# Performance work log

Hardware: AMD Instinct MI355X
Metric: run time of the kernel (lower is better)

Reference implementation:

```python
import jax, jax.numpy as jnp
import numpy as np

N_HEADS = 16


def setup_inputs() -> dict:
    key = jax.random.key(0)
    k1, k2 = jax.random.split(key)
    bs, width, length = 8, 3 * N_HEADS * 64, 1024  # C=64 per head
    qkv = jax.random.normal(k1, (bs, width, length), dtype=jnp.float32)
    mask = jax.random.uniform(k2, (bs, length), dtype=jnp.float32)
    return {"qkv": qkv, "mask": mask}


def reference(qkv, mask):
    bs, width, length = qkv.shape
    ch = width // (3 * N_HEADS)
    q, k, v = jnp.split(qkv, 3, axis=1)
    # view(bs*H, ch, T): head index is inner (b*H + h ordering)
    q = q.reshape(bs * N_HEADS, ch, length)
    k = k.reshape(bs * N_HEADS, ch, length)
    v = v.reshape(bs * N_HEADS, ch, length)
    scale = 1.0 / jnp.sqrt(jnp.sqrt(jnp.asarray(ch, dtype=qkv.dtype)))
    # [bs*H, T, T] score matrix
    weight = jnp.einsum('bct,bcs->bts', q * scale, k * scale)
    # torch mask.repeat(n_heads, 1) tiles the batch dim -> jnp.tile
    m = jnp.tile(mask, (N_HEADS, 1))[:, None, :]  # [bs*H, 1, T]
    weight = weight * m
    weight = jax.nn.softmax(weight.astype(jnp.float32), axis=-1).astype(weight.dtype)
    a = jnp.einsum('bts,bcs->bct', weight, v)  # [bs*H, ch, T]
    return a.reshape(bs, N_HEADS * ch, length)
```

## Files before the change

kernel.cpp:

```cpp
#include <hip/hip_runtime.h>
#include <stdint.h>
#include <math.h>

typedef float  f32x4  __attribute__((ext_vector_type(4)));
typedef __bf16 bf16x8 __attribute__((ext_vector_type(8)));
typedef __bf16 bf16x4 __attribute__((ext_vector_type(4)));

#define MFMA16(a, b, c) __builtin_amdgcn_mfma_f32_16x16x32_bf16((a), (b), (c), 0, 0, 0)
#define EXP2(x) __builtin_amdgcn_exp2f(x)

static constexpr int kT = 1024;

static constexpr int kTileEl = 4096;
static constexpr size_t kTensorEl    = (size_t)128 * 16 * kTileEl;
static constexpr size_t kTensorBytes = kTensorEl * 2;

static constexpr int kLS = 72;

__device__ inline void async16(const void* g, void* l) {
  __builtin_amdgcn_global_load_lds(
      (const __attribute__((address_space(1))) void*)g,
      (__attribute__((address_space(3))) void*)l, 16, 0, 0);
}

__global__ __launch_bounds__(256, 8)
void prepass(const float* __restrict__ qkv, const float* __restrict__ mask,
             __bf16* __restrict__ kh, __bf16* __restrict__ vh)
{
  __shared__ float ts[64 * 65];
  const int tid = threadIdx.x;
  const int bid = blockIdx.x, bh = bid >> 4, tile = bid & 15;
  const int b = bh >> 4, h = bh & 15, t0 = tile * 64;
  const float* __restrict__ kb = qkv + (size_t)(b * 3072 + 1024 + h * 64) * kT;
  const float* __restrict__ vb = qkv + (size_t)(b * 3072 + 2048 + h * 64) * kT;
  const float* __restrict__ mrow = mask + (size_t)(h & 7) * kT;
  const size_t tbase = ((size_t)bh * 16 + tile) * kTileEl;

  const int t4   = (tid & 15) * 4;
  const int crow = tid >> 4;
  const f32x4 m4 = *(const f32x4*)&mrow[t0 + t4];
  #pragma unroll
  for (int i = 0; i < 4; ++i) {
    const int c = i * 16 + crow;
    f32x4 k4 = *(const f32x4*)&kb[(size_t)c * kT + t0 + t4];
    k4 *= m4;
    *(f32x4*)&ts[c * 65 + t4] = k4;
  }
  __syncthreads();

  #pragma unroll
  for (int i = 0; i < 2; ++i) {
    const int p = i * 256 + tid;
    const int chunk = p >> 6, pl = p & 63;
    const int vc  = (chunk >> 1) * 16 + (pl & 15);
    const int vs0 = (chunk & 1) * 32 + (pl >> 4) * 8;
    const f32x4 va  = *(const f32x4*)&vb[(size_t)vc * kT + t0 + vs0];
    const f32x4 vbq = *(const f32x4*)&vb[(size_t)vc * kT + t0 + vs0 + 4];
    const int ks  = (chunk >> 1) * 16 + (pl & 15);
    const int kc0 = (chunk & 1) * 32 + (pl >> 4) * 8;
    bf16x8 k8, v8;
    #pragma unroll
    for (int j = 0; j < 8; ++j) k8[j] = (__bf16)ts[(kc0 + j) * 65 + ks];
    #pragma unroll
    for (int j = 0; j < 4; ++j) { v8[j] = (__bf16)va[j]; v8[4 + j] = (__bf16)vbq[j]; }
    *(bf16x8*)&kh[tbase + (size_t)p * 8] = k8;
    *(bf16x8*)&vh[tbase + (size_t)p * 8] = v8;
  }
}

__global__ __launch_bounds__(256, 5)
void attn_main(const float* __restrict__ qkv,
               const __bf16* __restrict__ kh, const __bf16* __restrict__ vh,
               float* __restrict__ out)
{
  __shared__ __align__(16) char smem[24576];

  const int tid  = threadIdx.x;
  const int lane = tid & 63;
  const int wave = tid >> 6;
  const int quad = lane >> 4;
  const int l15  = lane & 15;

  const int bid = blockIdx.x;
  const int bh  = bid & 127;
  const int tt  = bid >> 7;
  const int b   = bh >> 4;
  const int h   = bh & 15;
  const int t0  = tt * 64;
  const size_t hbase = (size_t)bh * 16;

  bf16x8 qh[2], ql[2];
  {
    float* ts = (float*)smem;
    const float* __restrict__ qb = qkv + (size_t)(b * 3072 + h * 64) * kT;
    const int t4   = (tid & 15) * 4;
    const int crow = tid >> 4;
    #pragma unroll
    for (int i = 0; i < 4; ++i) {
      const int c = i * 16 + crow;
      f32x4 q4 = *(const f32x4*)&qb[(size_t)c * kT + t0 + t4];
      q4 *= 0.18033688f;
      *(f32x4*)&ts[c * 65 + t4] = q4;
    }
    __syncthreads();
    const int trow = wave * 16 + l15;
    #pragma unroll
    for (int kc = 0; kc < 2; ++kc) {
      bf16x8 hf, lf;
      #pragma unroll
      for (int j = 0; j < 8; ++j) {
        float q = ts[(kc * 32 + quad * 8 + j) * 65 + trow];
        __bf16 hi = (__bf16)q;
        hf[j] = hi;
        lf[j] = (__bf16)(q - (float)hi);
      }
      qh[kc] = hf;
      ql[kc] = lf;
    }
    __syncthreads();
  }

  {
    const char* g = (const char*)(kh + hbase * kTileEl) + (size_t)lane * 16;
    for (int i = wave; i < 8; i += 4) async16(g + i * 1024, smem + i * 1024);
  }

  f32x4 O[4];
  #pragma unroll
  for (int cc = 0; cc < 4; ++cc) O[cc] = (f32x4){0.f, 0.f, 0.f, 0.f};
  float lsum = 0.f;

  char* sPw = smem + 16384 + wave * 2048;
  const int pwr = (l15 << 4) + ((quad & 1) << 3) + ((quad >> 1) << 8);

  for (int st = 0; st < 16; ++st) {
    __syncthreads();

    const __bf16* __restrict__ vt = vh + (hbase + st) * kTileEl;

    bf16x8 vf0[4], vf1[4];
    #pragma unroll
    for (int cc = 0; cc < 4; ++cc)
      vf0[cc] = *(const bf16x8*)&vt[(size_t)(cc * 2) * 512 + lane * 8];

    if (st < 15) {
      const char* g = (const char*)(kh + (hbase + st + 1) * kTileEl) + (size_t)lane * 16;
      char* l = smem + ((st + 1) & 1) * 8192;
      for (int i = wave; i < 8; i += 4) async16(g + i * 1024, l + i * 1024);
    }

    const __bf16* __restrict__ sKc = (const __bf16*)(smem + (st & 1) * 8192);

    #pragma unroll
    for (int sc = 0; sc < 4; ++sc) {
      bf16x8 k0 = *(const bf16x8*)&sKc[(size_t)(sc * 2) * 512 + lane * 8];
      bf16x8 k1 = *(const bf16x8*)&sKc[(size_t)(sc * 2 + 1) * 512 + lane * 8];
      f32x4 a = (f32x4){0.f, 0.f, 0.f, 0.f};
      a = MFMA16(k0, ql[0], a);
      a = MFMA16(k0, qh[0], a);
      a = MFMA16(k1, ql[1], a);
      a = MFMA16(k1, qh[1], a);
      bf16x4 p;
      #pragma unroll
      for (int r = 0; r < 4; ++r) {
        float e = EXP2(a[r]);
        lsum += e;
        p[r] = (__bf16)e;
      }
      *(bf16x4*)(sPw + (((sc >> 1) << 10) + ((sc & 1) << 9) + pwr)) = p;
    }

    #pragma unroll
    for (int cc = 0; cc < 4; ++cc)
      vf1[cc] = *(const bf16x8*)&vt[(size_t)(cc * 2 + 1) * 512 + lane * 8];

    bf16x8 pb0 = *(const bf16x8*)(sPw + lane * 16);
    bf16x8 pb1 = *(const bf16x8*)(sPw + 1024 + lane * 16);

    #pragma unroll
    for (int cc = 0; cc < 4; ++cc) {
      O[cc] = MFMA16(vf0[cc], pb0, O[cc]);
      O[cc] = MFMA16(vf1[cc], pb1, O[cc]);
    }
  }

  lsum += __shfl_xor(lsum, 16);
  lsum += __shfl_xor(lsum, 32);
  const float inv = 1.0f / lsum;

  const int tcol = t0 + wave * 16 + l15;
  float* __restrict__ obase = out + (size_t)b * (1024 * 1024) + (size_t)(h * 64) * kT;
  #pragma unroll
  for (int cc = 0; cc < 4; ++cc) {
    #pragma unroll
    for (int r = 0; r < 4; ++r) {
      obase[(size_t)(cc * 16 + quad * 4 + r) * kT + tcol] = O[cc][r] * inv;
    }
  }
}

__global__ __launch_bounds__(256, 2)
void attn_fused(const float* __restrict__ qkv, const float* __restrict__ mask,
                float* __restrict__ out)
{
  __shared__ __align__(16) __bf16 Ahi[64 * kLS];
  __shared__ __align__(16) __bf16 Alo[64 * kLS];
  __shared__ __align__(16) __bf16 Vhi[64 * kLS];
  __shared__ __align__(16) __bf16 Vlo[64 * kLS];
  __shared__ __align__(16) __bf16 Phi[64 * kLS];
  __shared__ __align__(16) __bf16 Plo[64 * kLS];
  __shared__ __align__(16) float  ms[64];

  const int tid  = threadIdx.x;
  const int lane = tid & 63;
  const int wave = tid >> 6;
  const int quad = lane >> 4;
  const int l15  = lane & 15;

  const int bid = blockIdx.x;
  const int bh  = bid >> 4;
  const int tb  = bid & 15;
  const int b   = bh >> 4;
  const int h   = bh & 15;
  const int t0  = tb * 64;

  const float* __restrict__ qbase = qkv + (size_t)(b * 3072 + h * 64) * kT;
  const float* __restrict__ kbase = qkv + (size_t)(b * 3072 + 1024 + h * 64) * kT;
  const float* __restrict__ vbase = qkv + (size_t)(b * 3072 + 2048 + h * 64) * kT;
  const float* __restrict__ mrow  = mask + (size_t)(h & 7) * kT;

  const int sl = tid & 63;
  const int cg = tid >> 6;

  #pragma unroll
  for (int i = 0; i < 16; ++i) {
    const int c = cg * 16 + i;
    float v  = qbase[(size_t)c * kT + t0 + sl] * 0.125f;
    __bf16 hi = (__bf16)v;
    Ahi[sl * kLS + c] = hi;
    Alo[sl * kLS + c] = (__bf16)(v - (float)hi);
  }
  __syncthreads();

  bf16x8 qh[2], ql[2];
  {
    const int row = (wave * 16 + l15) * kLS;
    #pragma unroll
    for (int kc = 0; kc < 2; ++kc) {
      qh[kc] = *(const bf16x8*)&Ahi[row + kc * 32 + quad * 8];
      ql[kc] = *(const bf16x8*)&Alo[row + kc * 32 + quad * 8];
    }
  }
  __syncthreads();

  f32x4 O[4];
  #pragma unroll
  for (int cc = 0; cc < 4; ++cc) O[cc] = (f32x4){0.f, 0.f, 0.f, 0.f};
  float m_run = -__builtin_inff();
  float l_run = 0.f;

  for (int s0 = 0; s0 < kT; s0 += 64) {
    #pragma unroll
    for (int i = 0; i < 16; ++i) {
      const int c = cg * 16 + i;
      float kv   = kbase[(size_t)c * kT + s0 + sl];
      __bf16 khi = (__bf16)kv;
      Ahi[sl * kLS + c] = khi;
      Alo[sl * kLS + c] = (__bf16)(kv - (float)khi);
      float vv   = vbase[(size_t)c * kT + s0 + sl];
      __bf16 vhi = (__bf16)vv;
      Vhi[c * kLS + sl] = vhi;
      Vlo[c * kLS + sl] = (__bf16)(vv - (float)vhi);
    }
    if (tid < 64) ms[tid] = mrow[s0 + tid];
    __syncthreads();

    f32x4 S[4];
    #pragma unroll
    for (int sc = 0; sc < 4; ++sc) {
      f32x4 acc = (f32x4){0.f, 0.f, 0.f, 0.f};
      #pragma unroll
      for (int kc = 0; kc < 2; ++kc) {
        const int off = (sc * 16 + l15) * kLS + kc * 32 + quad * 8;
        bf16x8 kh8 = *(const bf16x8*)&Ahi[off];
        bf16x8 kl8 = *(const bf16x8*)&Alo[off];
        acc = MFMA16(kh8, ql[kc], acc);
        acc = MFMA16(kl8, qh[kc], acc);
        acc = MFMA16(kh8, qh[kc], acc);
      }
      S[sc] = acc;
    }

    float x[16];
    float tmax = -__builtin_inff();
    #pragma unroll
    for (int sc = 0; sc < 4; ++sc) {
      f32x4 mv = *(const f32x4*)&ms[sc * 16 + quad * 4];
      #pragma unroll
      for (int r = 0; r < 4; ++r) {
        float xv = S[sc][r] * mv[r];
        x[sc * 4 + r] = xv;
        tmax = fmaxf(tmax, xv);
      }
    }
    tmax = fmaxf(tmax, __shfl_xor(tmax, 16));
    tmax = fmaxf(tmax, __shfl_xor(tmax, 32));
    const float mnew  = fmaxf(m_run, tmax);
    const float alpha = __expf(m_run - mnew);
    float tsum = 0.f;
    #pragma unroll
    for (int i = 0; i < 16; ++i) {
      float p = __expf(x[i] - mnew);
      x[i] = p;
      tsum += p;
    }
    tsum += __shfl_xor(tsum, 16);
    tsum += __shfl_xor(tsum, 32);
    l_run = l_run * alpha + tsum;
    m_run = mnew;
    #pragma unroll
    for (int cc = 0; cc < 4; ++cc) O[cc] = O[cc] * alpha;

    const int prow = (wave * 16 + l15) * kLS;
    #pragma unroll
    for (int sc = 0; sc < 4; ++sc) {
      bf16x4 ph, pl;
      #pragma unroll
      for (int r = 0; r < 4; ++r) {
        float p   = x[sc * 4 + r];
        __bf16 hi = (__bf16)p;
        ph[r] = hi;
        pl[r] = (__bf16)(p - (float)hi);
      }
      *(bf16x4*)&Phi[prow + sc * 16 + quad * 4] = ph;
      *(bf16x4*)&Plo[prow + sc * 16 + quad * 4] = pl;
    }
    __syncthreads();

    bf16x8 pbh[2], pbl[2];
    #pragma unroll
    for (int kc = 0; kc < 2; ++kc) {
      pbh[kc] = *(const bf16x8*)&Phi[prow + kc * 32 + quad * 8];
      pbl[kc] = *(const bf16x8*)&Plo[prow + kc * 32 + quad * 8];
    }
    #pragma unroll
    for (int cc = 0; cc < 4; ++cc) {
      #pragma unroll
      for (int kc = 0; kc < 2; ++kc) {
        const int off = (cc * 16 + l15) * kLS + kc * 32 + quad * 8;
        bf16x8 v8 = *(const bf16x8*)&Vhi[off];
        bf16x8 w8 = *(const bf16x8*)&Vlo[off];
        O[cc] = MFMA16(v8, pbl[kc], O[cc]);
        O[cc] = MFMA16(w8, pbh[kc], O[cc]);
        O[cc] = MFMA16(v8, pbh[kc], O[cc]);
      }
    }
    __syncthreads();
  }

  const float inv  = 1.0f / l_run;
  const int   tcol = t0 + wave * 16 + l15;
  float* __restrict__ obase = out + (size_t)b * (1024 * 1024) + (size_t)(h * 64) * kT;
  #pragma unroll
  for (int cc = 0; cc < 4; ++cc) {
    #pragma unroll
    for (int r = 0; r < 4; ++r) {
      const int c = cc * 16 + quad * 4 + r;
      obase[(size_t)c * kT + tcol] = O[cc][r] * inv;
    }
  }
}

extern "C" void kernel_launch(void* const* d_in, const int* in_sizes, int n_in,
                              void* d_out, int out_size, void* d_ws, size_t ws_size,
                              hipStream_t stream)
{
  const float* qkv  = (const float*)d_in[0];
  const float* mask = (const float*)d_in[1];
  float* out = (float*)d_out;
  (void)in_sizes; (void)n_in; (void)out_size;

  if (ws_size >= 2 * kTensorBytes) {
    char* w = (char*)d_ws;
    __bf16* kh = (__bf16*)(w + 0 * kTensorBytes);
    __bf16* vh = (__bf16*)(w + 1 * kTensorBytes);
    prepass<<<dim3(2048), dim3(256), 0, stream>>>(qkv, mask, kh, vh);
    attn_main<<<dim3(2048), dim3(256), 0, stream>>>(qkv, kh, vh, out);
  } else {
    attn_fused<<<dim3(2048), dim3(256), 0, stream>>>(qkv, mask, out);
  }
}
```

Baseline: 214.7 us.

## Process two 64-query tiles per block to reuse K/V loads

```diff
diff --git a/kernel.cpp b/kernel.cpp
--- a/kernel.cpp
+++ b/kernel.cpp
@@ -68,12 +68,12 @@
   }
 }
 
-__global__ __launch_bounds__(256, 5)
+__global__ __launch_bounds__(256, 4)
 void attn_main(const float* __restrict__ qkv,
                const __bf16* __restrict__ kh, const __bf16* __restrict__ vh,
                float* __restrict__ out)
 {
-  __shared__ __align__(16) char smem[24576];
+  __shared__ __align__(16) char smem[32768];
 
   const int tid  = threadIdx.x;
   const int lane = tid & 63;
@@ -83,41 +83,45 @@
 
   const int bid = blockIdx.x;
   const int bh  = bid & 127;
-  const int tt  = bid >> 7;
+  const int tp  = bid >> 7;
   const int b   = bh >> 4;
   const int h   = bh & 15;
-  const int t0  = tt * 64;
+  const int t0  = tp * 128;
   const size_t hbase = (size_t)bh * 16;
 
-  bf16x8 qh[2], ql[2];
+  bf16x8 qh[2][2], ql[2][2];
   {
     float* ts = (float*)smem;
     const float* __restrict__ qb = qkv + (size_t)(b * 3072 + h * 64) * kT;
     const int t4   = (tid & 15) * 4;
     const int crow = tid >> 4;
-    #pragma unroll
-    for (int i = 0; i < 4; ++i) {
-      const int c = i * 16 + crow;
-      f32x4 q4 = *(const f32x4*)&qb[(size_t)c * kT + t0 + t4];
-      q4 *= 0.18033688f;
-      *(f32x4*)&ts[c * 65 + t4] = q4;
-    }
-    __syncthreads();
     const int trow = wave * 16 + l15;
     #pragma unroll
-    for (int kc = 0; kc < 2; ++kc) {
-      bf16x8 hf, lf;
-      #pragma unroll
-      for (int j = 0; j < 8; ++j) {
-        float q = ts[(kc * 32 + quad * 8 + j) * 65 + trow];
-        __bf16 hi = (__bf16)q;
-        hf[j] = hi;
-        lf[j] = (__bf16)(q - (float)hi);
-      }
-      qh[kc] = hf;
-      ql[kc] = lf;
-    }
-    __syncthreads();
+    for (int half = 0; half < 2; ++half) {
+      const int tq0 = t0 + half * 64;
+      #pragma unroll
+      for (int i = 0; i < 4; ++i) {
+        const int c = i * 16 + crow;
+        f32x4 q4 = *(const f32x4*)&qb[(size_t)c * kT + tq0 + t4];
+        q4 *= 0.18033688f;
+        *(f32x4*)&ts[c * 65 + t4] = q4;
+      }
+      __syncthreads();
+      #pragma unroll
+      for (int kc = 0; kc < 2; ++kc) {
+        bf16x8 hf, lf;
+        #pragma unroll
+        for (int j = 0; j < 8; ++j) {
+          float q = ts[(kc * 32 + quad * 8 + j) * 65 + trow];
+          __bf16 hi = (__bf16)q;
+          hf[j] = hi;
+          lf[j] = (__bf16)(q - (float)hi);
+        }
+        qh[half][kc] = hf;
+        ql[half][kc] = lf;
+      }
+      __syncthreads();
+    }
   }
 
   {
@@ -125,12 +129,16 @@
     for (int i = wave; i < 8; i += 4) async16(g + i * 1024, smem + i * 1024);
   }
 
-  f32x4 O[4];
-  #pragma unroll
-  for (int cc = 0; cc < 4; ++cc) O[cc] = (f32x4){0.f, 0.f, 0.f, 0.f};
-  float lsum = 0.f;
-
-  char* sPw = smem + 16384 + wave * 2048;
+  f32x4 O0[4], O1[4];
+  #pragma unroll
+  for (int cc = 0; cc < 4; ++cc) {
+    O0[cc] = (f32x4){0.f, 0.f, 0.f, 0.f};
+    O1[cc] = (f32x4){0.f, 0.f, 0.f, 0.f};
+  }
+  float ls0 = 0.f, ls1 = 0.f;
+
+  char* sP0 = smem + 16384 + wave * 4096;
+  char* sP1 = sP0 + 2048;
   const int pwr = (l15 << 4) + ((quad & 1) << 3) + ((quad >> 1) << 8);
 
   for (int st = 0; st < 16; ++st) {
@@ -151,42 +159,63 @@
 
     const __bf16* __restrict__ sKc = (const __bf16*)(smem + (st & 1) * 8192);
 
+    __builtin_amdgcn_s_setprio(1);
+
     #pragma unroll
     for (int sc = 0; sc < 4; ++sc) {
       bf16x8 k0 = *(const bf16x8*)&sKc[(size_t)(sc * 2) * 512 + lane * 8];
       bf16x8 k1 = *(const bf16x8*)&sKc[(size_t)(sc * 2 + 1) * 512 + lane * 8];
-      f32x4 a = (f32x4){0.f, 0.f, 0.f, 0.f};
-      a = MFMA16(k0, ql[0], a);
-      a = MFMA16(k0, qh[0], a);
-      a = MFMA16(k1, ql[1], a);
-      a = MFMA16(k1, qh[1], a);
-      bf16x4 p;
+      f32x4 a0 = (f32x4){0.f, 0.f, 0.f, 0.f};
+      f32x4 a1 = (f32x4){0.f, 0.f, 0.f, 0.f};
+      a0 = MFMA16(k0, ql[0][0], a0);
+      a1 = MFMA16(k0, ql[1][0], a1);
+      a0 = MFMA16(k0, qh[0][0], a0);
+      a1 = MFMA16(k0, qh[1][0], a1);
+      a0 = MFMA16(k1, ql[0][1], a0);
+      a1 = MFMA16(k1, ql[1][1], a1);
+      a0 = MFMA16(k1, qh[0][1], a0);
+      a1 = MFMA16(k1, qh[1][1], a1);
+      bf16x4 p0, p1;
       #pragma unroll
       for (int r = 0; r < 4; ++r) {
-        float e = EXP2(a[r]);
-        lsum += e;
-        p[r] = (__bf16)e;
-      }
-      *(bf16x4*)(sPw + (((sc >> 1) << 10) + ((sc & 1) << 9) + pwr)) = p;
+        float e0 = EXP2(a0[r]);
+        float e1 = EXP2(a1[r]);
+        ls0 += e0;
+        ls1 += e1;
+        p0[r] = (__bf16)e0;
+        p1[r] = (__bf16)e1;
+      }
+      const int po = ((sc >> 1) << 10) + ((sc & 1) << 9) + pwr;
+      *(bf16x4*)(sP0 + po) = p0;
+      *(bf16x4*)(sP1 + po) = p1;
     }
 
     #pragma unroll
     for (int cc = 0; cc < 4; ++cc)
       vf1[cc] = *(const bf16x8*)&vt[(size_t)(cc * 2 + 1) * 512 + lane * 8];
 
-    bf16x8 pb0 = *(const bf16x8*)(sPw + lane * 16);
-    bf16x8 pb1 = *(const bf16x8*)(sPw + 1024 + lane * 16);
+    bf16x8 pb00 = *(const bf16x8*)(sP0 + lane * 16);
+    bf16x8 pb01 = *(const bf16x8*)(sP0 + 1024 + lane * 16);
+    bf16x8 pb10 = *(const bf16x8*)(sP1 + lane * 16);
+    bf16x8 pb11 = *(const bf16x8*)(sP1 + 1024 + lane * 16);
 
     #pragma unroll
     for (int cc = 0; cc < 4; ++cc) {
-      O[cc] = MFMA16(vf0[cc], pb0, O[cc]);
-      O[cc] = MFMA16(vf1[cc], pb1, O[cc]);
-    }
-  }
-
-  lsum += __shfl_xor(lsum, 16);
-  lsum += __shfl_xor(lsum, 32);
-  const float inv = 1.0f / lsum;
+      O0[cc] = MFMA16(vf0[cc], pb00, O0[cc]);
+      O1[cc] = MFMA16(vf0[cc], pb10, O1[cc]);
+      O0[cc] = MFMA16(vf1[cc], pb01, O0[cc]);
+      O1[cc] = MFMA16(vf1[cc], pb11, O1[cc]);
+    }
+
+    __builtin_amdgcn_s_setprio(0);
+  }
+
+  ls0 += __shfl_xor(ls0, 16);
+  ls0 += __shfl_xor(ls0, 32);
+  ls1 += __shfl_xor(ls1, 16);
+  ls1 += __shfl_xor(ls1, 32);
+  const float inv0 = 1.0f / ls0;
+  const float inv1 = 1.0f / ls1;
 
   const int tcol = t0 + wave * 16 + l15;
   float* __restrict__ obase = out + (size_t)b * (1024 * 1024) + (size_t)(h * 64) * kT;
@@ -194,7 +223,9 @@
   for (int cc = 0; cc < 4; ++cc) {
     #pragma unroll
     for (int r = 0; r < 4; ++r) {
-      obase[(size_t)(cc * 16 + quad * 4 + r) * kT + tcol] = O[cc][r] * inv;
+      const int c = cc * 16 + quad * 4 + r;
+      obase[(size_t)c * kT + tcol]      = O0[cc][r] * inv0;
+      obase[(size_t)c * kT + tcol + 64] = O1[cc][r] * inv1;
     }
   }
 }
@@ -385,7 +416,7 @@
     __bf16* kh = (__bf16*)(w + 0 * kTensorBytes);
     __bf16* vh = (__bf16*)(w + 1 * kTensorBytes);
     prepass<<<dim3(2048), dim3(256), 0, stream>>>(qkv, mask, kh, vh);
-    attn_main<<<dim3(2048), dim3(256), 0, stream>>>(qkv, kh, vh, out);
+    attn_main<<<dim3(1024), dim3(256), 0, stream>>>(qkv, kh, vh, out);
   } else {
     attn_fused<<<dim3(2048), dim3(256), 0, stream>>>(qkv, mask, out);
   }
```

New measurement: 212.0 us. About the same (-1.3%).
